# Kernel tuning notes

Hardware: AMD Instinct MI355X
Metric: run time of the kernel (lower is better)

The kernel has to match this reference:

```python
import jax, jax.numpy as jnp
import numpy as np

B, L, N, S, M = 4096, 512, 12, 128, 12


def setup_inputs() -> dict:
    key = jax.random.key(0)
    ks = jax.random.split(key, 8)
    sc = 1.0 / np.sqrt(S)
    scn = 1.0 / np.sqrt(N)
    return {
        "x": jax.random.normal(ks[0], (B, L, N), dtype=jnp.float32),
        "a0": jax.random.uniform(ks[1], (B, S), dtype=jnp.float32),
        "U_w": jax.random.uniform(ks[2], (N, S), minval=-scn, maxval=scn, dtype=jnp.float32),
        "U_b": jax.random.uniform(ks[3], (S,), minval=-scn, maxval=scn, dtype=jnp.float32),
        "W_w": jax.random.uniform(ks[4], (S, S), minval=-sc, maxval=sc, dtype=jnp.float32),
        "W_b": jax.random.uniform(ks[5], (S,), minval=-sc, maxval=sc, dtype=jnp.float32),
        "V_w": jax.random.uniform(ks[6], (S, M), minval=-sc, maxval=sc, dtype=jnp.float32),
        "V_b": jax.random.uniform(ks[7], (M,), minval=-sc, maxval=sc, dtype=jnp.float32),
    }


def reference(x, a0, U_w, U_b, W_w, W_b, V_w, V_b):
    # Elman RNN cell: a_t = relu(U(x_t) + W(a_{t-1})); output y = V(a_L)
    # Precompute input projection for all steps at once: [B,L,S]
    ux = jnp.einsum("bln,ns->bls", x, U_w) + U_b

    def step(a, ux_t):  # a: [B,S], ux_t: [B,S]
        a_new = jax.nn.relu(ux_t + a @ W_w + W_b)
        return a_new, None

    a_last, _ = jax.lax.scan(step, a0, jnp.swapaxes(ux, 0, 1))  # scan over L
    return a_last @ V_w + V_b  # [B, M]
```

## Files before the change

kernel.cpp:

```cpp
#include <hip/hip_runtime.h>
#include <hip/hip_bf16.h>

typedef __attribute__((ext_vector_type(8))) short bf16x8;
typedef __attribute__((ext_vector_type(4))) float f32x4;

#define L_SEQ 512
#define N_IN 12
#define S_DIM 128
#define M_OUT 12
#define LPAD 40
#define KT_STRIDE (16*LPAD)

__device__ inline short f2bf(float f) {
    union { float f; unsigned u; } q; q.f = f;
    unsigned r = (q.u + 0x7fffu + ((q.u >> 16) & 1u)) >> 16;
    return (short)r;
}
__device__ inline unsigned cvtpk(float lo, float hi) {
    unsigned r;
    asm("v_cvt_pk_bf16_f32 %0, %1, %2" : "=v"(r) : "v"(lo), "v"(hi));
    return r;
}
__device__ inline int s_perm(int kt, int q, int j) {
    return 32 * kt + 16 * (j >> 2) + 4 * q + (j & 3);
}
__device__ inline void block_sync() {
    asm volatile("s_waitcnt lgkmcnt(0)" ::: "memory");
    __builtin_amdgcn_s_barrier();
}

__global__ __launch_bounds__(512, 1)
void elman_kernel(const float* __restrict__ x,
                  const float* __restrict__ a0,
                  const float* __restrict__ U_w,
                  const float* __restrict__ U_b,
                  const float* __restrict__ W_w,
                  const float* __restrict__ W_b,
                  const float* __restrict__ V_w,
                  const float* __restrict__ V_b,
                  float* __restrict__ out)
{
    __shared__ __align__(16) short stx[2][4 * KT_STRIDE];
    __shared__ __align__(16) short xr[4][64 * 8];

    const int tid  = threadIdx.x;
    const int w    = tid >> 6;
    const int l    = tid & 63;
    const int n    = l & 15;
    const int q    = l >> 4;
    const bool qodd = (q & 1);
    const int b0   = blockIdx.x * 16;
    const int row  = b0 + n;
    const int fragoff = n * LPAD + q * 8;

    const float* xpA = x + (size_t)row * L_SEQ * N_IN + (q & 1) * 8;
    const float* xpB = xpA + (qodd ? 0 : 4);

#define MAKE_XF(XF, XA, XB) do {                                                       \
    union { unsigned uu[4]; bf16x8 v; } xu_;                                           \
    xu_.uu[0] = cvtpk(XA.x, XA.y);                                                     \
    xu_.uu[1] = cvtpk(XA.z, XA.w);                                                     \
    xu_.uu[2] = qodd ? 0x00003F80u : cvtpk(XB.x, XB.y);        \
    xu_.uu[3] = qodd ? 0u          : cvtpk(XB.z, XB.w);                                \
    XF = xu_.v;                                                                        \
} while (0)

    bf16x8 wf[2][4]; bf16x8 uf[2];
    if (w < 4) {
        #pragma unroll
        for (int h = 0; h < 2; ++h) {
            const int c = (2 * w + h) * 16 + n;
            #pragma unroll
            for (int li = 0; li < 4; ++li) {
                const int kt = (w + li) & 3;
                #pragma unroll
                for (int j = 0; j < 8; ++j)
                    wf[h][li][j] = f2bf(W_w[(size_t)s_perm(kt, q, j) * S_DIM + c]);
            }
            #pragma unroll
            for (int j = 0; j < 8; ++j) {
                const int k = q * 8 + j;
                float v;
                if (k < N_IN)       v = U_w[(size_t)k * S_DIM + c];
                else if (k == N_IN) v = W_b[c] + U_b[c];
                else                v = 0.f;
                uf[h][j] = f2bf(v);
            }
        }
    }

    for (int idx = tid; idx < 4 * 16 * 32; idx += 512) {
        const int kt = idx >> 9, r = (idx >> 5) & 15, qj = idx & 31;
        const int s = s_perm(kt, qj >> 3, qj & 7);
        stx[0][kt * KT_STRIDE + r * LPAD + qj] = f2bf(a0[(size_t)(b0 + r) * S_DIM + s]);
    }

    float4 xa, xb;
    if (w >= 4) {
        const int h = w & 3;
        if (h < 2) {
            float4 pa = *(const float4*)(xpA + (size_t)h * N_IN);
            float4 pb = *(const float4*)(xpB + (size_t)h * N_IN);
            bf16x8 xf; MAKE_XF(xf, pa, pb);
            *(bf16x8*)&xr[h][l * 8] = xf;
        }
        const int sf = ((h + 2) & 3) + 2;
        xa = *(const float4*)(xpA + (size_t)sf * N_IN);
        xb = *(const float4*)(xpB + (size_t)sf * N_IN);
    }
    block_sync();

    bf16x8 stOwn, stf1, stf2, stf3, xfc;
    f32x4 accU0, accU1;
    if (w < 4) {
        const short* rd = &stx[0][0];
        stOwn = *(const bf16x8*)&rd[((w + 0) & 3) * KT_STRIDE + fragoff];
        stf1  = *(const bf16x8*)&rd[((w + 1) & 3) * KT_STRIDE + fragoff];
        stf2  = *(const bf16x8*)&rd[((w + 2) & 3) * KT_STRIDE + fragoff];
        stf3  = *(const bf16x8*)&rd[((w + 3) & 3) * KT_STRIDE + fragoff];
        bf16x8 xf0 = *(const bf16x8*)&xr[0][l * 8];
        xfc        = *(const bf16x8*)&xr[1][l * 8];
        f32x4 z = {0.f, 0.f, 0.f, 0.f};
        accU0 = __builtin_amdgcn_mfma_f32_16x16x32_bf16(uf[0], xf0, z, 0, 0, 0);
        accU1 = __builtin_amdgcn_mfma_f32_16x16x32_bf16(uf[1], xf0, z, 0, 0, 0);
    }

    for (int t = 0; t < L_SEQ; t += 4) {
        #pragma unroll
        for (int u = 0; u < 4; ++u) {
            const int tt = t + u;
            if (w < 4) {
                f32x4 z = {0.f, 0.f, 0.f, 0.f};
                f32x4 c0a = __builtin_amdgcn_mfma_f32_16x16x32_bf16(wf[0][0], stOwn, accU0, 0, 0, 0);
                f32x4 c1a = __builtin_amdgcn_mfma_f32_16x16x32_bf16(wf[1][0], stOwn, accU1, 0, 0, 0);
                accU0 = __builtin_amdgcn_mfma_f32_16x16x32_bf16(uf[0], xfc, z, 0, 0, 0);
                accU1 = __builtin_amdgcn_mfma_f32_16x16x32_bf16(uf[1], xfc, z, 0, 0, 0);
                c0a = __builtin_amdgcn_mfma_f32_16x16x32_bf16(wf[0][1], stf1, c0a, 0, 0, 0);
                c1a = __builtin_amdgcn_mfma_f32_16x16x32_bf16(wf[1][1], stf1, c1a, 0, 0, 0);
                f32x4 c0b = __builtin_amdgcn_mfma_f32_16x16x32_bf16(wf[0][2], stf2, z, 0, 0, 0);
                f32x4 c1b = __builtin_amdgcn_mfma_f32_16x16x32_bf16(wf[1][2], stf2, z, 0, 0, 0);
                c0b = __builtin_amdgcn_mfma_f32_16x16x32_bf16(wf[0][3], stf3, c0b, 0, 0, 0);
                c1b = __builtin_amdgcn_mfma_f32_16x16x32_bf16(wf[1][3], stf3, c1b, 0, 0, 0);
                union { unsigned uu[4]; bf16x8 v; } su;
                su.uu[0] = cvtpk(fmaxf(c0a[0] + c0b[0], 0.f), fmaxf(c0a[1] + c0b[1], 0.f));
                su.uu[1] = cvtpk(fmaxf(c0a[2] + c0b[2], 0.f), fmaxf(c0a[3] + c0b[3], 0.f));
                su.uu[2] = cvtpk(fmaxf(c1a[0] + c1b[0], 0.f), fmaxf(c1a[1] + c1b[1], 0.f));
                su.uu[3] = cvtpk(fmaxf(c1a[2] + c1b[2], 0.f), fmaxf(c1a[3] + c1b[3], 0.f));
                stOwn = su.v;
                *(bf16x8*)&stx[(tt + 1) & 1][w * KT_STRIDE + fragoff] = stOwn;
            } else {
                if ((w & 3) == ((u + 2) & 3)) {
                    bf16x8 xf; MAKE_XF(xf, xa, xb);
                    *(bf16x8*)&xr[(tt + 2) & 3][l * 8] = xf;
                    const int s2 = (tt + 6 < L_SEQ) ? (tt + 6) : (L_SEQ - 1);
                    xa = *(const float4*)(xpA + (size_t)s2 * N_IN);
                    xb = *(const float4*)(xpB + (size_t)s2 * N_IN);
                }
            }
            block_sync();
            if (w < 4) {
                const short* rd = &stx[(tt + 1) & 1][0];
                stf1 = *(const bf16x8*)&rd[((w + 1) & 3) * KT_STRIDE + fragoff];
                stf2 = *(const bf16x8*)&rd[((w + 2) & 3) * KT_STRIDE + fragoff];
                stf3 = *(const bf16x8*)&rd[((w + 3) & 3) * KT_STRIDE + fragoff];
                xfc  = *(const bf16x8*)&xr[(tt + 2) & 3][l * 8];
            }
        }
    }

    if (w == 0) {
        f32x4 acc = {0.f, 0.f, 0.f, 0.f};
        #pragma unroll
        for (int li = 0; li < 4; ++li) {
            bf16x8 vf;
            #pragma unroll
            for (int j = 0; j < 8; ++j)
                vf[j] = (n < M_OUT)
                      ? f2bf(V_w[(size_t)s_perm(li, q, j) * M_OUT + n])
                      : (short)0;
            const bf16x8 stt = (li == 0) ? stOwn : (li == 1) ? stf1 : (li == 2) ? stf2 : stf3;
            acc = __builtin_amdgcn_mfma_f32_16x16x32_bf16(vf, stt, acc, 0, 0, 0);
        }
        #pragma unroll
        for (int j = 0; j < 4; ++j) {
            const int m = 4 * q + j;
            if (m < M_OUT)
                out[(size_t)row * M_OUT + m] = acc[j] + V_b[m];
        }
    }
#undef MAKE_XF
}

extern "C" void kernel_launch(void* const* d_in, const int* in_sizes, int n_in,
                              void* d_out, int out_size, void* d_ws, size_t ws_size,
                              hipStream_t stream) {
    const float* x   = (const float*)d_in[0];
    const float* a0  = (const float*)d_in[1];
    const float* U_w = (const float*)d_in[2];
    const float* U_b = (const float*)d_in[3];
    const float* W_w = (const float*)d_in[4];
    const float* W_b = (const float*)d_in[5];
    const float* V_w = (const float*)d_in[6];
    const float* V_b = (const float*)d_in[7];
    float* out = (float*)d_out;

    hipLaunchKernelGGL(elman_kernel, dim3(4096 / 16), dim3(512), 0, stream,
                       x, a0, U_w, U_b, W_w, W_b, V_w, V_b, out);
}
```

Measured before the change: 122.1 us.

## Move input-projection MFMAs to producer waves and raise recurrent wave priority

The U·x input projection MFMAs move off the four recurrent waves and onto the four helper waves. The helpers convert x, run the projection, and write fp32 accumulators into a 4-deep shared ring. The recurrent waves then only load the precomputed accumulators and run the W·h chain, wrapped in s_setprio to favour the critical path. This shortens the per-step serial critical path, at the cost of more LDS traffic and more shared memory. All four helper waves now work every step instead of one per step.

```diff
diff --git a/kernel.cpp b/kernel.cpp
--- a/kernel.cpp
+++ b/kernel.cpp
@@ -41,7 +41,7 @@
                   float* __restrict__ out)
 {
     __shared__ __align__(16) short stx[2][4 * KT_STRIDE];
-    __shared__ __align__(16) short xr[4][64 * 8];
+    __shared__ __align__(16) float aux[4][4][2][64][4];
 
     const int tid  = threadIdx.x;
     const int w    = tid >> 6;
@@ -52,6 +52,7 @@
     const int b0   = blockIdx.x * 16;
     const int row  = b0 + n;
     const int fragoff = n * LPAD + q * 8;
+    const int hw   = w & 3;
 
     const float* xpA = x + (size_t)row * L_SEQ * N_IN + (q & 1) * 8;
     const float* xpB = xpA + (qodd ? 0 : 4);
@@ -77,6 +78,11 @@
                 for (int j = 0; j < 8; ++j)
                     wf[h][li][j] = f2bf(W_w[(size_t)s_perm(kt, q, j) * S_DIM + c]);
             }
+        }
+    } else {
+        #pragma unroll
+        for (int h = 0; h < 2; ++h) {
+            const int c = (2 * hw + h) * 16 + n;
             #pragma unroll
             for (int j = 0; j < 8; ++j) {
                 const int k = q * 8 + j;
@@ -95,22 +101,26 @@
         stx[0][kt * KT_STRIDE + r * LPAD + qj] = f2bf(a0[(size_t)(b0 + r) * S_DIM + s]);
     }
 
-    float4 xa, xb;
+    float4 x0A, x0B, x1A, x1B, x2A, x2B, x3A, x3B;
     if (w >= 4) {
-        const int h = w & 3;
-        if (h < 2) {
-            float4 pa = *(const float4*)(xpA + (size_t)h * N_IN);
-            float4 pb = *(const float4*)(xpB + (size_t)h * N_IN);
-            bf16x8 xf; MAKE_XF(xf, pa, pb);
-            *(bf16x8*)&xr[h][l * 8] = xf;
-        }
-        const int sf = ((h + 2) & 3) + 2;
-        xa = *(const float4*)(xpA + (size_t)sf * N_IN);
-        xb = *(const float4*)(xpB + (size_t)sf * N_IN);
+        float4 paA = *(const float4*)(xpA + 0 * N_IN), paB = *(const float4*)(xpB + 0 * N_IN);
+        float4 pbA = *(const float4*)(xpA + 1 * N_IN), pbB = *(const float4*)(xpB + 1 * N_IN);
+        x2A = *(const float4*)(xpA + 2 * N_IN); x2B = *(const float4*)(xpB + 2 * N_IN);
+        x3A = *(const float4*)(xpA + 3 * N_IN); x3B = *(const float4*)(xpB + 3 * N_IN);
+        x0A = *(const float4*)(xpA + 4 * N_IN); x0B = *(const float4*)(xpB + 4 * N_IN);
+        x1A = *(const float4*)(xpA + 5 * N_IN); x1B = *(const float4*)(xpB + 5 * N_IN);
+        f32x4 z = {0.f, 0.f, 0.f, 0.f};
+        bf16x8 xf;
+        MAKE_XF(xf, paA, paB);
+        *(f32x4*)&aux[0][hw][0][l][0] = __builtin_amdgcn_mfma_f32_16x16x32_bf16(uf[0], xf, z, 0, 0, 0);
+        *(f32x4*)&aux[0][hw][1][l][0] = __builtin_amdgcn_mfma_f32_16x16x32_bf16(uf[1], xf, z, 0, 0, 0);
+        MAKE_XF(xf, pbA, pbB);
+        *(f32x4*)&aux[1][hw][0][l][0] = __builtin_amdgcn_mfma_f32_16x16x32_bf16(uf[0], xf, z, 0, 0, 0);
+        *(f32x4*)&aux[1][hw][1][l][0] = __builtin_amdgcn_mfma_f32_16x16x32_bf16(uf[1], xf, z, 0, 0, 0);
     }
     block_sync();
 
-    bf16x8 stOwn, stf1, stf2, stf3, xfc;
+    bf16x8 stOwn, stf1, stf2, stf3;
     f32x4 accU0, accU1;
     if (w < 4) {
         const short* rd = &stx[0][0];
@@ -118,55 +128,62 @@
         stf1  = *(const bf16x8*)&rd[((w + 1) & 3) * KT_STRIDE + fragoff];
         stf2  = *(const bf16x8*)&rd[((w + 2) & 3) * KT_STRIDE + fragoff];
         stf3  = *(const bf16x8*)&rd[((w + 3) & 3) * KT_STRIDE + fragoff];
-        bf16x8 xf0 = *(const bf16x8*)&xr[0][l * 8];
-        xfc        = *(const bf16x8*)&xr[1][l * 8];
-        f32x4 z = {0.f, 0.f, 0.f, 0.f};
-        accU0 = __builtin_amdgcn_mfma_f32_16x16x32_bf16(uf[0], xf0, z, 0, 0, 0);
-        accU1 = __builtin_amdgcn_mfma_f32_16x16x32_bf16(uf[1], xf0, z, 0, 0, 0);
-    }
+        accU0 = *(const f32x4*)&aux[0][w][0][l][0];
+        accU1 = *(const f32x4*)&aux[0][w][1][l][0];
+    }
+
+#define STEP(PXA, PXB, UU) do {                                                        \
+    const int tt = t + (UU);                                                           \
+    if (w < 4) {                                                                       \
+        __builtin_amdgcn_s_setprio(1);                                                 \
+        f32x4 z = {0.f, 0.f, 0.f, 0.f};                                                \
+        f32x4 c0a = __builtin_amdgcn_mfma_f32_16x16x32_bf16(wf[0][0], stOwn, accU0, 0, 0, 0); \
+        f32x4 c1a = __builtin_amdgcn_mfma_f32_16x16x32_bf16(wf[1][0], stOwn, accU1, 0, 0, 0); \
+        c0a = __builtin_amdgcn_mfma_f32_16x16x32_bf16(wf[0][1], stf1, c0a, 0, 0, 0);   \
+        c1a = __builtin_amdgcn_mfma_f32_16x16x32_bf16(wf[1][1], stf1, c1a, 0, 0, 0);   \
+        f32x4 c0b = __builtin_amdgcn_mfma_f32_16x16x32_bf16(wf[0][2], stf2, z, 0, 0, 0); \
+        f32x4 c1b = __builtin_amdgcn_mfma_f32_16x16x32_bf16(wf[1][2], stf2, z, 0, 0, 0); \
+        c0b = __builtin_amdgcn_mfma_f32_16x16x32_bf16(wf[0][3], stf3, c0b, 0, 0, 0);   \
+        c1b = __builtin_amdgcn_mfma_f32_16x16x32_bf16(wf[1][3], stf3, c1b, 0, 0, 0);   \
+        union { unsigned uu[4]; bf16x8 v; } su;                                        \
+        su.uu[0] = cvtpk(fmaxf(c0a[0] + c0b[0], 0.f), fmaxf(c0a[1] + c0b[1], 0.f));    \
+        su.uu[1] = cvtpk(fmaxf(c0a[2] + c0b[2], 0.f), fmaxf(c0a[3] + c0b[3], 0.f));    \
+        su.uu[2] = cvtpk(fmaxf(c1a[0] + c1b[0], 0.f), fmaxf(c1a[1] + c1b[1], 0.f));    \
+        su.uu[3] = cvtpk(fmaxf(c1a[2] + c1b[2], 0.f), fmaxf(c1a[3] + c1b[3], 0.f));    \
+        stOwn = su.v;                                                                  \
+        *(bf16x8*)&stx[((UU) + 1) & 1][w * KT_STRIDE + fragoff] = stOwn;               \
+        __builtin_amdgcn_s_setprio(0);                                                 \
+    } else {                                                                           \
+              \
+        bf16x8 xf_; MAKE_XF(xf_, PXA, PXB);                                            \
+        f32x4 z_ = {0.f, 0.f, 0.f, 0.f};                                               \
+        f32x4 u0_ = __builtin_amdgcn_mfma_f32_16x16x32_bf16(uf[0], xf_, z_, 0, 0, 0);  \
+        f32x4 u1_ = __builtin_amdgcn_mfma_f32_16x16x32_bf16(uf[1], xf_, z_, 0, 0, 0);  \
+        *(f32x4*)&aux[((UU) + 2) & 3][hw][0][l][0] = u0_;                              \
+        *(f32x4*)&aux[((UU) + 2) & 3][hw][1][l][0] = u1_;                              \
+        const int s2_ = (tt + 6 < L_SEQ) ? (tt + 6) : (L_SEQ - 1);                     \
+        PXA = *(const float4*)(xpA + (size_t)s2_ * N_IN);                              \
+        PXB = *(const float4*)(xpB + (size_t)s2_ * N_IN);                              \
+    }                                                                                  \
+    block_sync();                                                                      \
+    if (w < 4) {                                                                       \
+        const short* rd_ = &stx[((UU) + 1) & 1][0];                                    \
+        stf1 = *(const bf16x8*)&rd_[((w + 1) & 3) * KT_STRIDE + fragoff];              \
+        stf2 = *(const bf16x8*)&rd_[((w + 2) & 3) * KT_STRIDE + fragoff];              \
+        stf3 = *(const bf16x8*)&rd_[((w + 3) & 3) * KT_STRIDE + fragoff];              \
+        accU0 = *(const f32x4*)&aux[((UU) + 1) & 3][w][0][l][0];                       \
+        accU1 = *(const f32x4*)&aux[((UU) + 1) & 3][w][1][l][0];                       \
+    }                                                                                  \
+} while (0)
 
     for (int t = 0; t < L_SEQ; t += 4) {
-        #pragma unroll
-        for (int u = 0; u < 4; ++u) {
-            const int tt = t + u;
-            if (w < 4) {
-                f32x4 z = {0.f, 0.f, 0.f, 0.f};
-                f32x4 c0a = __builtin_amdgcn_mfma_f32_16x16x32_bf16(wf[0][0], stOwn, accU0, 0, 0, 0);
-                f32x4 c1a = __builtin_amdgcn_mfma_f32_16x16x32_bf16(wf[1][0], stOwn, accU1, 0, 0, 0);
-                accU0 = __builtin_amdgcn_mfma_f32_16x16x32_bf16(uf[0], xfc, z, 0, 0, 0);
-                accU1 = __builtin_amdgcn_mfma_f32_16x16x32_bf16(uf[1], xfc, z, 0, 0, 0);
-                c0a = __builtin_amdgcn_mfma_f32_16x16x32_bf16(wf[0][1], stf1, c0a, 0, 0, 0);
-                c1a = __builtin_amdgcn_mfma_f32_16x16x32_bf16(wf[1][1], stf1, c1a, 0, 0, 0);
-                f32x4 c0b = __builtin_amdgcn_mfma_f32_16x16x32_bf16(wf[0][2], stf2, z, 0, 0, 0);
-                f32x4 c1b = __builtin_amdgcn_mfma_f32_16x16x32_bf16(wf[1][2], stf2, z, 0, 0, 0);
-                c0b = __builtin_amdgcn_mfma_f32_16x16x32_bf16(wf[0][3], stf3, c0b, 0, 0, 0);
-                c1b = __builtin_amdgcn_mfma_f32_16x16x32_bf16(wf[1][3], stf3, c1b, 0, 0, 0);
-                union { unsigned uu[4]; bf16x8 v; } su;
-                su.uu[0] = cvtpk(fmaxf(c0a[0] + c0b[0], 0.f), fmaxf(c0a[1] + c0b[1], 0.f));
-                su.uu[1] = cvtpk(fmaxf(c0a[2] + c0b[2], 0.f), fmaxf(c0a[3] + c0b[3], 0.f));
-                su.uu[2] = cvtpk(fmaxf(c1a[0] + c1b[0], 0.f), fmaxf(c1a[1] + c1b[1], 0.f));
-                su.uu[3] = cvtpk(fmaxf(c1a[2] + c1b[2], 0.f), fmaxf(c1a[3] + c1b[3], 0.f));
-                stOwn = su.v;
-                *(bf16x8*)&stx[(tt + 1) & 1][w * KT_STRIDE + fragoff] = stOwn;
-            } else {
-                if ((w & 3) == ((u + 2) & 3)) {
-                    bf16x8 xf; MAKE_XF(xf, xa, xb);
-                    *(bf16x8*)&xr[(tt + 2) & 3][l * 8] = xf;
-                    const int s2 = (tt + 6 < L_SEQ) ? (tt + 6) : (L_SEQ - 1);
-                    xa = *(const float4*)(xpA + (size_t)s2 * N_IN);
-                    xb = *(const float4*)(xpB + (size_t)s2 * N_IN);
-                }
-            }
-            block_sync();
-            if (w < 4) {
-                const short* rd = &stx[(tt + 1) & 1][0];
-                stf1 = *(const bf16x8*)&rd[((w + 1) & 3) * KT_STRIDE + fragoff];
-                stf2 = *(const bf16x8*)&rd[((w + 2) & 3) * KT_STRIDE + fragoff];
-                stf3 = *(const bf16x8*)&rd[((w + 3) & 3) * KT_STRIDE + fragoff];
-                xfc  = *(const bf16x8*)&xr[(tt + 2) & 3][l * 8];
-            }
-        }
-    }
+        STEP(x2A, x2B, 0);
+        STEP(x3A, x3B, 1);
+        STEP(x0A, x0B, 2);
+        STEP(x1A, x1B, 3);
+    }
+#undef STEP
+#undef MAKE_XF
 
     if (w == 0) {
         f32x4 acc = {0.f, 0.f, 0.f, 0.f};
@@ -188,7 +205,6 @@
                 out[(size_t)row * M_OUT + m] = acc[j] + V_b[m];
         }
     }
-#undef MAKE_XF
 }
 
 extern "C" void kernel_launch(void* const* d_in, const int* in_sizes, int n_in,
```

New measurement: 175.1 us. 1.43x slower.
